# Kernel optimization log

Measured on AMD Instinct MI355X. Metric: run time of the kernel, lower is better.

The kernel has to match this reference:

```python
import jax, jax.numpy as jnp
import numpy as np

B, C, S = 4, 2, 4096          # batch, in_channels, samples
K, NK, OUT = 64, 32, 512      # kernel_size, num_kernels, out_channels


def setup_inputs() -> dict:
    key = jax.random.key(0)
    k1, k2, k3, k4 = jax.random.split(key, 4)
    x = jax.random.normal(k1, (B, C, S), dtype=jnp.float32)
    # LearnableSTFTFunction.learnable_weights: (num_kernels, kernel_size), torch.randn init
    stft_w = jax.random.normal(k2, (NK, K), dtype=jnp.float32)
    # Conv1d(in=C*K*NK, out=OUT, kernel=1): weight (OUT, C*K*NK), bias (OUT,)
    conv_w = jax.random.normal(k3, (OUT, C * K * NK), dtype=jnp.float32) * 0.02
    conv_b = jax.random.normal(k4, (OUT,), dtype=jnp.float32) * 0.02
    return {"x": x, "stft_w": stft_w, "conv_w": conv_w, "conv_b": conv_b}


def reference(x, stft_w, conv_w, conv_b):
    b, c, s = x.shape
    nk, k = stft_w.shape
    # F.pad(x, (0, K-1)) then unfold(-1, K, 1) -> (b, c, s, K) sliding windows
    xp = jnp.pad(x, ((0, 0), (0, 0), (0, k - 1)))
    idx = jnp.arange(s)[:, None] + jnp.arange(k)[None, :]  # (s, K)
    win = xp[:, :, idx]  # (b, c, s, K)
    # einsum('ijklm,lm->ijkml') with l=1 broadcast: elementwise per-kernel weighting,
    # no reduction over m -> (b, c, s, K, NK)
    xw = jnp.einsum('bcsm,lm->bcsml', win, stft_w)
    # torch raw reshape (row-major), deliberately mixing s into channel blocks
    xr = xw.reshape(b, c * k * nk, s)
    # 1x1 Conv1d == channel matmul, then ReLU
    out = jnp.einsum('bis,oi->bos', xr, conv_w) + conv_b[None, :, None]
    return jax.nn.relu(out)
```

## Files before the change

### kernel.cpp

```cpp
#include <hip/hip_runtime.h>

#define NB   4
#define NC   2
#define NS   4096
#define NKW  64
#define NL   32
#define NOUT 512

__device__ __forceinline__ int sw(int i) { return i + (i >> 5); }

constexpr int XS_PHYS = 4290;
constexpr int WS_PHYS = 4224;

__global__ __launch_bounds__(256, 3)
void fused_cnn(const float* __restrict__ x,
               const float* __restrict__ stft_w,
               const float* __restrict__ conv_w,
               const float* __restrict__ conv_b,
               float* __restrict__ out)
{
    __shared__ float xs[NC * XS_PHYS];
    __shared__ float ws[WS_PHYS];
    __shared__ float Hs[65];

    const int tid = threadIdx.x;
    const int bid = blockIdx.x;
    const int b = bid >> 9;
    const int o = bid & 511;

    for (int c = 0; c < NC; ++c) {
        const float* xb = x + (size_t)(b * NC + c) * NS;
        float* dst = xs + c * XS_PHYS;
        #pragma unroll
        for (int it = 0; it < 4; ++it) {
            int i0 = (it * 256 + tid) * 4;
            float4 v = *(const float4*)(xb + i0);
            dst[sw(i0 + 0)] = v.x;
            dst[sw(i0 + 1)] = v.y;
            dst[sw(i0 + 2)] = v.z;
            dst[sw(i0 + 3)] = v.w;
        }
        if (tid < 64) dst[sw(4096 + tid)] = 0.0f;
    }
    {
        const float* wrow = conv_w + (size_t)o * 4096;
        #pragma unroll
        for (int it = 0; it < 4; ++it) {
            int i0 = (it * 256 + tid) * 4;
            float4 v = *(const float4*)(wrow + i0);
            ws[sw(i0 + 0)] = v.x;
            ws[sw(i0 + 1)] = v.y;
            ws[sw(i0 + 2)] = v.z;
            ws[sw(i0 + 3)] = v.w;
        }
    }
    __syncthreads();

    const int wave = tid >> 6;
    const int lane = tid & 63;
    const int u0 = wave << 4;

    float acc[17];
    #pragma unroll
    for (int i = 0; i < 17; ++i) acc[i] = 0.0f;

    for (int g = 0; g < 8; ++g) {
        int G = lane + (g << 6);
        int c = G >> 8;
        int t0 = (G & 255) << 3;
        int wb = c * 2048 + t0;
        float w[8];
        #pragma unroll
        for (int j = 0; j < 8; ++j) w[j] = ws[sw(wb + j)];
        const float* xc = xs + c * XS_PHYS;
        int xb0 = 2 * t0 + u0;
        #pragma unroll
        for (int d = 0; d <= 30; ++d) {
            float xv = xc[sw(xb0 + d)];
            #pragma unroll
            for (int j = 0; j < 8; ++j) {
                int uu = d - 2 * j;
                if (uu >= 0 && uu < 17)
                    acc[uu] += w[j] * xv;
            }
        }
    }

    #pragma unroll
    for (int uu = 0; uu < 17; ++uu) {
        float v = acc[uu];
        #pragma unroll
        for (int off = 1; off < 64; off <<= 1)
            v += __shfl_xor(v, off, 64);
        acc[uu] = v;
    }
    if (lane == 0) {
        #pragma unroll
        for (int uu = 0; uu < 17; ++uu) {
            if (uu < 16 || wave == 3)
                Hs[u0 + uu] = acc[uu];
        }
    }
    __syncthreads();

    const float bias = conv_b[o];
    float* ob = out + (size_t)(b * NOUT + o) * NS;
    #pragma unroll
    for (int it = 0; it < 4; ++it) {
        int s4 = (it * 256 + tid) * 4;
        int r = s4 >> 11;
        int q = s4 & 2047;
        int m = q >> 5;
        int l = q & 31;
        float h = Hs[r + m];
        float v0 = fmaf(stft_w[(l + 0) * NKW + m], h, bias);
        float v1 = fmaf(stft_w[(l + 1) * NKW + m], h, bias);
        float v2 = fmaf(stft_w[(l + 2) * NKW + m], h, bias);
        float v3 = fmaf(stft_w[(l + 3) * NKW + m], h, bias);
        float4 res;
        res.x = v0 > 0.0f ? v0 : 0.0f;
        res.y = v1 > 0.0f ? v1 : 0.0f;
        res.z = v2 > 0.0f ? v2 : 0.0f;
        res.w = v3 > 0.0f ? v3 : 0.0f;
        *(float4*)(ob + s4) = res;
    }
}

extern "C" void kernel_launch(void* const* d_in, const int* in_sizes, int n_in,
                              void* d_out, int out_size, void* d_ws, size_t ws_size,
                              hipStream_t stream) {
    const float* x      = (const float*)d_in[0];
    const float* stft_w = (const float*)d_in[1];
    const float* conv_w = (const float*)d_in[2];
    const float* conv_b = (const float*)d_in[3];
    float* out = (float*)d_out;
    fused_cnn<<<dim3(NB * NOUT), dim3(256), 0, stream>>>(x, stft_w, conv_w, conv_b, out);
}
```

Baseline: 106.4 us.

## Split reduction into bf16 MFMA split-K GEMM plus reduce-epilogue kernel

Replaces the single fused kernel, which did scalar FP32 FMAs per output channel, with two kernels. The first casts the conv weights and a Toeplitz-staged input to bf16 and computes the 65 H values per output channel with 32x32x16 MFMA, split along K into partial sums stored in the workspace. The second kernel reduces those partials and writes the broadcast epilogue. This moves the reduction onto matrix cores and trades precision (bf16 inputs) and an extra launch plus a workspace round trip for much higher arithmetic throughput.

```diff
diff --git a/kernel.cpp b/kernel.cpp
--- a/kernel.cpp
+++ b/kernel.cpp
@@ -1,105 +1,128 @@
 #include <hip/hip_runtime.h>
+#include <hip/hip_bf16.h>
 
 #define NB   4
 #define NC   2
 #define NS   4096
-#define NKW  64
-#define NL   32
 #define NOUT 512
+#define UPAD 80
+#define MT   128
 
-__device__ __forceinline__ int sw(int i) { return i + (i >> 5); }
+typedef short  short8_t  __attribute__((ext_vector_type(8)));
+typedef float  float16_t __attribute__((ext_vector_type(16)));
 
-constexpr int XS_PHYS = 4290;
-constexpr int WS_PHYS = 4224;
+__device__ __forceinline__ short bf16s(float f) {
+    union { __hip_bfloat16 b; short s; } u;
+    u.b = __float2bfloat16(f);
+    return u.s;
+}
 
-__global__ __launch_bounds__(256, 3)
-void fused_cnn(const float* __restrict__ x,
-               const float* __restrict__ stft_w,
-               const float* __restrict__ conv_w,
-               const float* __restrict__ conv_b,
-               float* __restrict__ out)
+template<int KCN>
+__global__ __launch_bounds__(256)
+void gemm_partials(const float* __restrict__ x,
+                   const float* __restrict__ conv_w,
+                   float* __restrict__ hpart)
 {
-    __shared__ float xs[NC * XS_PHYS];
-    __shared__ float ws[WS_PHYS];
-    __shared__ float Hs[65];
+    constexpr int KC  = 4096 / KCN;
+    constexpr int XSZ = KC + 56;
+    __shared__ __align__(16) short xS[16][XSZ];
+
+    const int blk = blockIdx.x;
+    const int kc  = blk % KCN;
+    const int ot  = (blk / KCN) & 3;
+    const int b   = blk / (KCN * 4);
+
+    const int K0 = kc * KC;
+    const int c  = K0 >> 11;
+    const int tb = K0 & 2047;
 
     const int tid = threadIdx.x;
-    const int bid = blockIdx.x;
-    const int b = bid >> 9;
-    const int o = bid & 511;
+    const float* xc = x + (size_t)(b * NC + c) * NS;
 
-    for (int c = 0; c < NC; ++c) {
-        const float* xb = x + (size_t)(b * NC + c) * NS;
-        float* dst = xs + c * XS_PHYS;
+    for (int i = tid; i < XSZ; i += 256) {
+        int ge = (tb + i) * 2;
+        float fe = (ge     < NS) ? xc[ge]     : 0.0f;
+        float fo = (ge + 1 < NS) ? xc[ge + 1] : 0.0f;
+        short se = bf16s(fe), so = bf16s(fo);
         #pragma unroll
-        for (int it = 0; it < 4; ++it) {
-            int i0 = (it * 256 + tid) * 4;
-            float4 v = *(const float4*)(xb + i0);
-            dst[sw(i0 + 0)] = v.x;
-            dst[sw(i0 + 1)] = v.y;
-            dst[sw(i0 + 2)] = v.z;
-            dst[sw(i0 + 3)] = v.w;
-        }
-        if (tid < 64) dst[sw(4096 + tid)] = 0.0f;
-    }
-    {
-        const float* wrow = conv_w + (size_t)o * 4096;
-        #pragma unroll
-        for (int it = 0; it < 4; ++it) {
-            int i0 = (it * 256 + tid) * 4;
-            float4 v = *(const float4*)(wrow + i0);
-            ws[sw(i0 + 0)] = v.x;
-            ws[sw(i0 + 1)] = v.y;
-            ws[sw(i0 + 2)] = v.z;
-            ws[sw(i0 + 3)] = v.w;
+        for (int r = 0; r < 8; ++r) {
+            int j = i - r;
+            if (j >= 0) { xS[r][j] = se; xS[8 + r][j] = so; }
         }
     }
     __syncthreads();
 
     const int wave = tid >> 6;
     const int lane = tid & 63;
-    const int u0 = wave << 4;
+    const int l31  = lane & 31;
+    const int q    = lane >> 5;
+    const int kq   = q * 8;
 
-    float acc[17];
+    const float* wrow = conv_w + (size_t)(ot * MT + wave * 32 + l31) * 4096 + K0;
+
+    float16_t acc[3];
     #pragma unroll
-    for (int i = 0; i < 17; ++i) acc[i] = 0.0f;
+    for (int nt = 0; nt < 3; ++nt)
+        #pragma unroll
+        for (int e = 0; e < 16; ++e) acc[nt][e] = 0.0f;
 
-    for (int g = 0; g < 8; ++g) {
-        int G = lane + (g << 6);
-        int c = G >> 8;
-        int t0 = (G & 255) << 3;
-        int wb = c * 2048 + t0;
-        float w[8];
+    int arr[3], hb[3];
+    #pragma unroll
+    for (int nt = 0; nt < 3; ++nt) {
+        int uu = nt * 32 + l31;
+        int h  = uu >> 1;
+        arr[nt] = (uu & 1) * 8 + (h & 7);
+        hb[nt]  = h & ~7;
+    }
+
+    #pragma unroll 4
+    for (int step = 0; step < KC / 16; ++step) {
+        const int kl = step * 16 + kq;
+        float4 a0 = *(const float4*)(wrow + kl);
+        float4 a1 = *(const float4*)(wrow + kl + 4);
+        short8_t af = { bf16s(a0.x), bf16s(a0.y), bf16s(a0.z), bf16s(a0.w),
+                        bf16s(a1.x), bf16s(a1.y), bf16s(a1.z), bf16s(a1.w) };
         #pragma unroll
-        for (int j = 0; j < 8; ++j) w[j] = ws[sw(wb + j)];
-        const float* xc = xs + c * XS_PHYS;
-        int xb0 = 2 * t0 + u0;
-        #pragma unroll
-        for (int d = 0; d <= 30; ++d) {
-            float xv = xc[sw(xb0 + d)];
+        for (int nt = 0; nt < 3; ++nt) {
+            short8_t bf = *(const short8_t*)&xS[arr[nt]][kl + hb[nt]];
+            acc[nt] = __builtin_amdgcn_mfma_f32_32x32x16_bf16(af, bf, acc[nt], 0, 0, 0);
+        }
+    }
+
+    float* hp = hpart + (size_t)(kc * NB + b) * NOUT * UPAD;
+    #pragma unroll
+    for (int nt = 0; nt < 3; ++nt) {
+        int uu = nt * 32 + l31;
+        if (uu < UPAD) {
             #pragma unroll
-            for (int j = 0; j < 8; ++j) {
-                int uu = d - 2 * j;
-                if (uu >= 0 && uu < 17)
-                    acc[uu] += w[j] * xv;
+            for (int reg = 0; reg < 16; ++reg) {
+                int row = (reg & 3) + 8 * (reg >> 2) + 4 * q;
+                int o   = ot * MT + wave * 32 + row;
+                hp[(size_t)o * UPAD + uu] = acc[nt][reg];
             }
         }
     }
+}
 
-    #pragma unroll
-    for (int uu = 0; uu < 17; ++uu) {
-        float v = acc[uu];
+template<int KCN>
+__global__ __launch_bounds__(256)
+void reduce_epilogue(const float* __restrict__ hpart,
+                     const float* __restrict__ stft_w,
+                     const float* __restrict__ conv_b,
+                     float* __restrict__ out)
+{
+    __shared__ float Hs[65];
+    const int tid = threadIdx.x;
+    const int bid = blockIdx.x;
+    const int b = bid >> 9;
+    const int o = bid & 511;
+
+    if (tid < 65) {
+        float h = 0.0f;
         #pragma unroll
-        for (int off = 1; off < 64; off <<= 1)
-            v += __shfl_xor(v, off, 64);
-        acc[uu] = v;
-    }
-    if (lane == 0) {
-        #pragma unroll
-        for (int uu = 0; uu < 17; ++uu) {
-            if (uu < 16 || wave == 3)
-                Hs[u0 + uu] = acc[uu];
-        }
+        for (int s = 0; s < KCN; ++s)
+            h += hpart[((size_t)(s * NB + b) * NOUT + o) * UPAD + tid];
+        Hs[tid] = h;
     }
     __syncthreads();
 
@@ -108,15 +131,15 @@
     #pragma unroll
     for (int it = 0; it < 4; ++it) {
         int s4 = (it * 256 + tid) * 4;
-        int r = s4 >> 11;
-        int q = s4 & 2047;
-        int m = q >> 5;
-        int l = q & 31;
+        int r  = s4 >> 11;
+        int qq = s4 & 2047;
+        int m  = qq >> 5;
+        int l  = qq & 31;
         float h = Hs[r + m];
-        float v0 = fmaf(stft_w[(l + 0) * NKW + m], h, bias);
-        float v1 = fmaf(stft_w[(l + 1) * NKW + m], h, bias);
-        float v2 = fmaf(stft_w[(l + 2) * NKW + m], h, bias);
-        float v3 = fmaf(stft_w[(l + 3) * NKW + m], h, bias);
+        float v0 = fmaf(stft_w[(l + 0) * 64 + m], h, bias);
+        float v1 = fmaf(stft_w[(l + 1) * 64 + m], h, bias);
+        float v2 = fmaf(stft_w[(l + 2) * 64 + m], h, bias);
+        float v3 = fmaf(stft_w[(l + 3) * 64 + m], h, bias);
         float4 res;
         res.x = v0 > 0.0f ? v0 : 0.0f;
         res.y = v1 > 0.0f ? v1 : 0.0f;
@@ -124,6 +147,14 @@
         res.w = v3 > 0.0f ? v3 : 0.0f;
         *(float4*)(ob + s4) = res;
     }
+}
+
+template<int KCN>
+static void launch_pair(const float* x, const float* stft_w, const float* conv_w,
+                        const float* conv_b, float* out, float* ws, hipStream_t stream)
+{
+    gemm_partials<KCN><<<dim3(NB * 4 * KCN), dim3(256), 0, stream>>>(x, conv_w, ws);
+    reduce_epilogue<KCN><<<dim3(NB * NOUT), dim3(256), 0, stream>>>(ws, stft_w, conv_b, out);
 }
 
 extern "C" void kernel_launch(void* const* d_in, const int* in_sizes, int n_in,
@@ -134,5 +165,11 @@
     const float* conv_w = (const float*)d_in[2];
     const float* conv_b = (const float*)d_in[3];
     float* out = (float*)d_out;
-    fused_cnn<<<dim3(NB * NOUT), dim3(256), 0, stream>>>(x, stft_w, conv_w, conv_b, out);
+    float* ws  = (float*)d_ws;
+
+    const size_t per_slice = (size_t)NB * NOUT * UPAD * sizeof(float);
+    if      (ws_size >= 16 * per_slice) launch_pair<16>(x, stft_w, conv_w, conv_b, out, ws, stream);
+    else if (ws_size >=  8 * per_slice) launch_pair<8>(x, stft_w, conv_w, conv_b, out, ws, stream);
+    else if (ws_size >=  4 * per_slice) launch_pair<4 >(x, stft_w, conv_w, conv_b, out, ws, stream);
+    else                                launch_pair<2 >(x, stft_w, conv_w, conv_b, out, ws, stream);
 }
```

Measured after the change: 88.43 us. -16.9%, faster.
